# Kernel tuning notes

Hardware: AMD Instinct MI355X
Metric: run time of the kernel (lower is better)

The kernel has to match this reference:

```python
import jax, jax.numpy as jnp
import numpy as np

TOKENS, D_MODEL, N_EXPERTS, K = 16384, 4096, 64, 2


def setup_inputs() -> dict:
    key = jax.random.key(0)
    kx, kw, kb = jax.random.split(key, 3)
    x = jax.random.normal(kx, (TOKENS, D_MODEL), dtype=jnp.float32)
    # nn.Linear(input_dim, num_experts): weight [num_experts, input_dim], bias [num_experts]
    bound = 1.0 / np.sqrt(D_MODEL)
    W = jax.random.uniform(kw, (N_EXPERTS, D_MODEL), minval=-bound, maxval=bound, dtype=jnp.float32)
    b = jax.random.uniform(kb, (N_EXPERTS,), minval=-bound, maxval=bound, dtype=jnp.float32)
    return {"x": x, "W": W, "b": b}


def reference(x, W, b):
    # logits = x @ W.T + b ; softmax over experts ; top-k
    logits = jnp.einsum('td,ed->te', x, W) + b  # [tokens, experts]
    scores = jax.nn.softmax(logits, axis=-1)
    topk_scores, topk_indices = jax.lax.top_k(scores, K)
    return (topk_indices, topk_scores)
```

## Files before the change

### kernel.cpp

```cpp
#include <hip/hip_runtime.h>
#include <hip/hip_bf16.h>
#include <cstdint>
#include <cstddef>

#define TOKENS 16384
#define DMODEL 4096
#define NEXP   64
#define NWAVE  4
#define KSPAN  (DMODEL / NWAVE)
#define NKC    (KSPAN / 16)
#define NMAC   (NKC / 4)

typedef __attribute__((ext_vector_type(8)))  short bf16x8;
typedef __attribute__((ext_vector_type(16))) float f32x16;

__device__ __forceinline__ void cvt_hilo8(const float f[8], bf16x8* hi, bf16x8* lo) {
  union { __hip_bfloat16 b; unsigned short u; } cv;
  bf16x8 hv, lv;
#pragma unroll
  for (int j = 0; j < 8; ++j) {
    __hip_bfloat16 hb = __float2bfloat16(f[j]);
    cv.b = hb; hv[j] = (short)cv.u;
    float r = f[j] - __bfloat162float(hb);
    cv.b = __float2bfloat16(r); lv[j] = (short)cv.u;
  }
  *hi = hv; *lo = lv;
}

__global__ __launch_bounds__(256)
void prep_W(const float* __restrict__ W, uint4* __restrict__ wh, uint4* __restrict__ wl) {
  const int tid = blockIdx.x * 256 + threadIdx.x;
  const int l  = tid & 63;
  const int et = (tid >> 6) & 1;
  const int kc = tid >> 7;
  const int e  = et * 32 + (l & 31);
  const int k  = kc * 16 + (l >> 5) * 8;
  const float* src = W + (size_t)e * DMODEL + k;
  float f[8];
#pragma unroll
  for (int j = 0; j < 8; ++j) f[j] = src[j];
  bf16x8 hi, lo;
  cvt_hilo8(f, &hi, &lo);
  const int slot = (kc * 2 + et) * 64 + l;
  wh[slot] = __builtin_bit_cast(uint4, hi);
  wl[slot] = __builtin_bit_cast(uint4, lo);
}

__global__ __launch_bounds__(256, 2)
void gemm_topk(const float* __restrict__ x, const uint4* __restrict__ wh,
               const uint4* __restrict__ wl, const float* __restrict__ b,
               float* __restrict__ out) {
  __shared__ float red[NWAVE][32 * NEXP];

  const int tid = threadIdx.x;
  const int l   = tid & 63;
  const int w   = tid >> 6;
  const int t0  = blockIdx.x * 32;
  const int row = l & 31, g = l >> 5;
  const int ph  = blockIdx.x & 15;

  const float* xp  = x  + (size_t)(t0 + row) * DMODEL + w * KSPAN + g * 8;
  const uint4* whp = wh + (size_t)w * (NKC * 128) + l;
  const uint4* wlp = wl + (size_t)w * (NKC * 128) + l;

  auto rot = [&](int kc) { return ((((kc >> 2) + ph) & 15) << 2) | (kc & 3); };

  f32x16 acc0, acc1;
#pragma unroll
  for (int i = 0; i < 16; ++i) { acc0[i] = 0.f; acc1[i] = 0.f; }

  float4 xa[2][8];
  uint4  ph0[2], ph1[2], pl0[2], pl1[2];

  auto ldxm = [&](int mac, int s) {
    const int rm = (mac + ph) & 15;
#pragma unroll
    for (int c = 0; c < 4; ++c) {
      const float* xn = xp + (size_t)(rm * 4 + c) * 16;
      xa[s][c * 2]     = *(const float4*)(xn);
      xa[s][c * 2 + 1] = *(const float4*)(xn + 4);
    }
  };
  auto ldw = [&](int kc, int s) {
    const int rc = rot(kc);
    ph0[s] = whp[rc * 128];  ph1[s] = whp[rc * 128 + 64];
    pl0[s] = wlp[rc * 128];  pl1[s] = wlp[rc * 128 + 64];
  };

  auto chunk = [&](int kc, int xs, int c) {
    const int ws = kc & 1;
    float4 a0 = xa[xs][c * 2], a1 = xa[xs][c * 2 + 1];
    uint4 bh0 = ph0[ws], bh1 = ph1[ws], bl0 = pl0[ws], bl1 = pl1[ws];
    if (kc + 2 < NKC) ldw(kc + 2, ws);
    float f[8] = {a0.x, a0.y, a0.z, a0.w, a1.x, a1.y, a1.z, a1.w};
    bf16x8 ah, al;
    cvt_hilo8(f, &ah, &al);
    bf16x8 vh0 = __builtin_bit_cast(bf16x8, bh0);
    bf16x8 vh1 = __builtin_bit_cast(bf16x8, bh1);
    bf16x8 vl0 = __builtin_bit_cast(bf16x8, bl0);
    bf16x8 vl1 = __builtin_bit_cast(bf16x8, bl1);
    acc0 = __builtin_amdgcn_mfma_f32_32x32x16_bf16(ah, vh0, acc0, 0, 0, 0);
    acc1 = __builtin_amdgcn_mfma_f32_32x32x16_bf16(ah, vh1, acc1, 0, 0, 0);
    acc0 = __builtin_amdgcn_mfma_f32_32x32x16_bf16(ah, vl0, acc0, 0, 0, 0);
    acc1 = __builtin_amdgcn_mfma_f32_32x32x16_bf16(ah, vl1, acc1, 0, 0, 0);
    acc0 = __builtin_amdgcn_mfma_f32_32x32x16_bf16(al, vh0, acc0, 0, 0, 0);
    acc1 = __builtin_amdgcn_mfma_f32_32x32x16_bf16(al, vh1, acc1, 0, 0, 0);
  };

  ldxm(0, 0);
  ldw(0, 0); ldw(1, 1);

  for (int m = 0; m < NMAC; m += 2) {
    if (m + 1 < NMAC) ldxm(m + 1, 1);
#pragma unroll
    for (int c = 0; c < 4; ++c) chunk(m * 4 + c, 0, c);
    if (m + 2 < NMAC) ldxm(m + 2, 0);
#pragma unroll
    for (int c = 0; c < 4; ++c) chunk((m + 1) * 4 + c, 1, c);
  }

  {
    float* rp = &red[w][0];
#pragma unroll
    for (int r = 0; r < 16; ++r) {
      const int rr = (r & 3) + 8 * (r >> 2) + 4 * g;
      rp[rr * NEXP + row]      = acc0[r];
      rp[rr * NEXP + 32 + row] = acc1[r];
    }
  }
  __syncthreads();

  const float bias = b[tid & 63];
#pragma unroll
  for (int j = 0; j < 8; ++j) {
    const int f = tid + 256 * j;
    float s = red[0][f] + red[1][f] + red[2][f] + red[3][f] + bias;
    red[0][f] = s;
  }
  __syncthreads();

#pragma unroll
  for (int i = 0; i < 8; ++i) {
    const int tl = w * 8 + i;
    const float v = red[0][tl * NEXP + l];

    float m1 = v; int i1 = l;
#pragma unroll
    for (int off = 32; off > 0; off >>= 1) {
      float ov = __shfl_xor(m1, off, 64);
      int   oi = __shfl_xor(i1, off, 64);
      if (ov > m1 || (ov == m1 && oi < i1)) { m1 = ov; i1 = oi; }
    }
    float v2 = (l == i1) ? -__builtin_inff() : v;
    float m2 = v2; int i2 = l;
#pragma unroll
    for (int off = 32; off > 0; off >>= 1) {
      float ov = __shfl_xor(m2, off, 64);
      int   oi = __shfl_xor(i2, off, 64);
      if (ov > m2 || (ov == m2 && oi < i2)) { m2 = ov; i2 = oi; }
    }
    float e = __expf(v - m1);
#pragma unroll
    for (int off = 32; off > 0; off >>= 1) e += __shfl_xor(e, off, 64);

    if (l == 0) {
      const int t = t0 + tl;
      out[(size_t)t * 2 + 0] = (float)i1;
      out[(size_t)t * 2 + 1] = (float)i2;
      float inv = 1.0f / e;
      out[(size_t)TOKENS * 2 + (size_t)t * 2 + 0] = inv;
      out[(size_t)TOKENS * 2 + (size_t)t * 2 + 1] = __expf(m2 - m1) * inv;
    }
  }
}

extern "C" void kernel_launch(void* const* d_in, const int* in_sizes, int n_in,
                              void* d_out, int out_size, void* d_ws, size_t ws_size,
                              hipStream_t stream) {
  const float* x = (const float*)d_in[0];
  const float* W = (const float*)d_in[1];
  const float* b = (const float*)d_in[2];
  float* out = (float*)d_out;

  uint4* wh = (uint4*)d_ws;
  uint4* wl = wh + 32768;

  hipLaunchKernelGGL(prep_W,    dim3(128),         dim3(256), 0, stream, W, wh, wl);
  hipLaunchKernelGGL(gemm_topk, dim3(TOKENS / 32), dim3(256), 0, stream, x, wh, wl, b, out);
}
```

Measured before the change: 77.71 us.

## Process 64 tokens per block with 8 waves to reuse W fragments

Each block now covers 64 tokens with 8 waves, each wave handling half the K span. Every wave computes two 32-token tiles against the same loaded W hi/lo fragments, which halves W fragment traffic per token. The per-block rotation of the K order is removed. The reduction buffer grows to 128KB of LDS, so only one block fits per CU, and the cross-wave reduction now sums 8 partials.

```diff
diff --git a/kernel.cpp b/kernel.cpp
--- a/kernel.cpp
+++ b/kernel.cpp
@@ -6,10 +6,10 @@
 #define TOKENS 16384
 #define DMODEL 4096
 #define NEXP   64
-#define NWAVE  4
+#define NWAVE  8
 #define KSPAN  (DMODEL / NWAVE)
 #define NKC    (KSPAN / 16)
-#define NMAC   (NKC / 4)
+#define NMAC   (NKC / 2)
 
 typedef __attribute__((ext_vector_type(8)))  short bf16x8;
 typedef __attribute__((ext_vector_type(16))) float f32x16;
@@ -46,65 +46,76 @@
   wl[slot] = __builtin_bit_cast(uint4, lo);
 }
 
-__global__ __launch_bounds__(256, 2)
+__global__ __launch_bounds__(512, 2)
 void gemm_topk(const float* __restrict__ x, const uint4* __restrict__ wh,
                const uint4* __restrict__ wl, const float* __restrict__ b,
                float* __restrict__ out) {
-  __shared__ float red[NWAVE][32 * NEXP];
+  __shared__ float red[NWAVE][64 * NEXP];
 
   const int tid = threadIdx.x;
   const int l   = tid & 63;
   const int w   = tid >> 6;
-  const int t0  = blockIdx.x * 32;
+  const int t0  = blockIdx.x * 64;
   const int row = l & 31, g = l >> 5;
-  const int ph  = blockIdx.x & 15;
-
-  const float* xp  = x  + (size_t)(t0 + row) * DMODEL + w * KSPAN + g * 8;
+
+  const float* xpA = x + (size_t)(t0 + row) * DMODEL + w * KSPAN + g * 8;
+  const float* xpB = xpA + (size_t)32 * DMODEL;
   const uint4* whp = wh + (size_t)w * (NKC * 128) + l;
   const uint4* wlp = wl + (size_t)w * (NKC * 128) + l;
 
-  auto rot = [&](int kc) { return ((((kc >> 2) + ph) & 15) << 2) | (kc & 3); };
-
-  f32x16 acc0, acc1;
-#pragma unroll
-  for (int i = 0; i < 16; ++i) { acc0[i] = 0.f; acc1[i] = 0.f; }
+  f32x16 accA0, accA1, accB0, accB1;
+#pragma unroll
+  for (int i = 0; i < 16; ++i) { accA0[i] = 0.f; accA1[i] = 0.f; accB0[i] = 0.f; accB1[i] = 0.f; }
 
   float4 xa[2][8];
   uint4  ph0[2], ph1[2], pl0[2], pl1[2];
 
   auto ldxm = [&](int mac, int s) {
-    const int rm = (mac + ph) & 15;
-#pragma unroll
-    for (int c = 0; c < 4; ++c) {
-      const float* xn = xp + (size_t)(rm * 4 + c) * 16;
+#pragma unroll
+    for (int c = 0; c < 2; ++c) {
+      const float* xn = xpA + (size_t)(mac * 2 + c) * 16;
       xa[s][c * 2]     = *(const float4*)(xn);
       xa[s][c * 2 + 1] = *(const float4*)(xn + 4);
     }
+#pragma unroll
+    for (int c = 0; c < 2; ++c) {
+      const float* xn = xpB + (size_t)(mac * 2 + c) * 16;
+      xa[s][4 + c * 2]     = *(const float4*)(xn);
+      xa[s][4 + c * 2 + 1] = *(const float4*)(xn + 4);
+    }
   };
   auto ldw = [&](int kc, int s) {
-    const int rc = rot(kc);
-    ph0[s] = whp[rc * 128];  ph1[s] = whp[rc * 128 + 64];
-    pl0[s] = wlp[rc * 128];  pl1[s] = wlp[rc * 128 + 64];
+    ph0[s] = whp[(size_t)kc * 128];  ph1[s] = whp[(size_t)kc * 128 + 64];
+    pl0[s] = wlp[(size_t)kc * 128];  pl1[s] = wlp[(size_t)kc * 128 + 64];
   };
 
   auto chunk = [&](int kc, int xs, int c) {
     const int ws = kc & 1;
-    float4 a0 = xa[xs][c * 2], a1 = xa[xs][c * 2 + 1];
+    float4 aA0 = xa[xs][c * 2],     aA1 = xa[xs][c * 2 + 1];
+    float4 aB0 = xa[xs][4 + c * 2], aB1 = xa[xs][4 + c * 2 + 1];
     uint4 bh0 = ph0[ws], bh1 = ph1[ws], bl0 = pl0[ws], bl1 = pl1[ws];
     if (kc + 2 < NKC) ldw(kc + 2, ws);
-    float f[8] = {a0.x, a0.y, a0.z, a0.w, a1.x, a1.y, a1.z, a1.w};
-    bf16x8 ah, al;
-    cvt_hilo8(f, &ah, &al);
+    float fA[8] = {aA0.x, aA0.y, aA0.z, aA0.w, aA1.x, aA1.y, aA1.z, aA1.w};
+    float fB[8] = {aB0.x, aB0.y, aB0.z, aB0.w, aB1.x, aB1.y, aB1.z, aB1.w};
+    bf16x8 ahA, alA, ahB, alB;
+    cvt_hilo8(fA, &ahA, &alA);
+    cvt_hilo8(fB, &ahB, &alB);
     bf16x8 vh0 = __builtin_bit_cast(bf16x8, bh0);
     bf16x8 vh1 = __builtin_bit_cast(bf16x8, bh1);
     bf16x8 vl0 = __builtin_bit_cast(bf16x8, bl0);
     bf16x8 vl1 = __builtin_bit_cast(bf16x8, bl1);
-    acc0 = __builtin_amdgcn_mfma_f32_32x32x16_bf16(ah, vh0, acc0, 0, 0, 0);
-    acc1 = __builtin_amdgcn_mfma_f32_32x32x16_bf16(ah, vh1, acc1, 0, 0, 0);
-    acc0 = __builtin_amdgcn_mfma_f32_32x32x16_bf16(ah, vl0, acc0, 0, 0, 0);
-    acc1 = __builtin_amdgcn_mfma_f32_32x32x16_bf16(ah, vl1, acc1, 0, 0, 0);
-    acc0 = __builtin_amdgcn_mfma_f32_32x32x16_bf16(al, vh0, acc0, 0, 0, 0);
-    acc1 = __builtin_amdgcn_mfma_f32_32x32x16_bf16(al, vh1, acc1, 0, 0, 0);
+    accA0 = __builtin_amdgcn_mfma_f32_32x32x16_bf16(ahA, vh0, accA0, 0, 0, 0);
+    accA1 = __builtin_amdgcn_mfma_f32_32x32x16_bf16(ahA, vh1, accA1, 0, 0, 0);
+    accB0 = __builtin_amdgcn_mfma_f32_32x32x16_bf16(ahB, vh0, accB0, 0, 0, 0);
+    accB1 = __builtin_amdgcn_mfma_f32_32x32x16_bf16(ahB, vh1, accB1, 0, 0, 0);
+    accA0 = __builtin_amdgcn_mfma_f32_32x32x16_bf16(ahA, vl0, accA0, 0, 0, 0);
+    accA1 = __builtin_amdgcn_mfma_f32_32x32x16_bf16(ahA, vl1, accA1, 0, 0, 0);
+    accB0 = __builtin_amdgcn_mfma_f32_32x32x16_bf16(ahB, vl0, accB0, 0, 0, 0);
+    accB1 = __builtin_amdgcn_mfma_f32_32x32x16_bf16(ahB, vl1, accB1, 0, 0, 0);
+    accA0 = __builtin_amdgcn_mfma_f32_32x32x16_bf16(alA, vh0, accA0, 0, 0, 0);
+    accA1 = __builtin_amdgcn_mfma_f32_32x32x16_bf16(alA, vh1, accA1, 0, 0, 0);
+    accB0 = __builtin_amdgcn_mfma_f32_32x32x16_bf16(alB, vh0, accB0, 0, 0, 0);
+    accB1 = __builtin_amdgcn_mfma_f32_32x32x16_bf16(alB, vh1, accB1, 0, 0, 0);
   };
 
   ldxm(0, 0);
@@ -112,11 +123,9 @@
 
   for (int m = 0; m < NMAC; m += 2) {
     if (m + 1 < NMAC) ldxm(m + 1, 1);
-#pragma unroll
-    for (int c = 0; c < 4; ++c) chunk(m * 4 + c, 0, c);
+    chunk(m * 2, 0, 0);  chunk(m * 2 + 1, 0, 1);
     if (m + 2 < NMAC) ldxm(m + 2, 0);
-#pragma unroll
-    for (int c = 0; c < 4; ++c) chunk((m + 1) * 4 + c, 1, c);
+    chunk((m + 1) * 2, 1, 0);  chunk((m + 1) * 2 + 1, 1, 1);
   }
 
   {
@@ -124,8 +133,10 @@
 #pragma unroll
     for (int r = 0; r < 16; ++r) {
       const int rr = (r & 3) + 8 * (r >> 2) + 4 * g;
-      rp[rr * NEXP + row]      = acc0[r];
-      rp[rr * NEXP + 32 + row] = acc1[r];
+      rp[rr * NEXP + row]             = accA0[r];
+      rp[rr * NEXP + 32 + row]        = accA1[r];
+      rp[(32 + rr) * NEXP + row]      = accB0[r];
+      rp[(32 + rr) * NEXP + 32 + row] = accB1[r];
     }
   }
   __syncthreads();
@@ -133,8 +144,9 @@
   const float bias = b[tid & 63];
 #pragma unroll
   for (int j = 0; j < 8; ++j) {
-    const int f = tid + 256 * j;
-    float s = red[0][f] + red[1][f] + red[2][f] + red[3][f] + bias;
+    const int f = tid + 512 * j;
+    float s = red[0][f] + red[1][f] + red[2][f] + red[3][f]
+            + red[4][f] + red[5][f] + red[6][f] + red[7][f] + bias;
     red[0][f] = s;
   }
   __syncthreads();
@@ -186,5 +198,5 @@
   uint4* wl = wh + 32768;
 
   hipLaunchKernelGGL(prep_W,    dim3(128),         dim3(256), 0, stream, W, wh, wl);
-  hipLaunchKernelGGL(gemm_topk, dim3(TOKENS / 32), dim3(256), 0, stream, x, wh, wl, b, out);
-}
+  hipLaunchKernelGGL(gemm_topk, dim3(TOKENS / 64), dim3(512), 0, stream, x, wh, wl, b, out);
+}
```

Result: faster. 75.24 us (median of 2 runs) (-3.2%).
